# Performance work log

Measured on AMD Instinct MI355X. Metric: run time of the kernel, lower is better.

## Reference

```python
import jax, jax.numpy as jnp
import numpy as np

B, T, NB = 8, 120, 40
VD, WD = 2053, 300
H, E, NH, HD = 512, 256, 8, 64
SEG, NSEG = 12, 10
IDX = np.round(np.linspace(SEG - 1, T - 1, NSEG)).astype(int)  # segment endpoints


def setup_inputs():
    keys = iter(jax.random.split(jax.random.key(0), 64))
    def w(*shape):
        return jax.random.normal(next(keys), shape, jnp.float32) * 0.02
    z = lambda *s: jnp.zeros(s, jnp.float32)
    return dict(
        videos=jax.random.normal(next(keys), (B, T, NB, VD), jnp.float32),
        sub_glove=jax.random.normal(next(keys), (B, WD), jnp.float32),
        obj_glove=jax.random.normal(next(keys), (B, WD), jnp.float32),
        W_ev=w(VD - 5, E), b_ev=z(E),
        W_el=w(5, E), b_el=z(E),
        W_ew=w(WD, E), b_ew=z(E),
        W_sp1=w(2 * E, E), b_sp1=z(E), w_sp2=w(E),
        W_s2o=w(NB, E), b_s2o=z(E),
        W_o2s=w(NB, E), b_o2s=z(E),
        W_tv=w(H, H), b_tv=z(H),
        Wq=w(H, H), bq=z(H), Wk=w(H, H), bk=z(H), Wv=w(H, H), bv=z(H), Wo=w(H, H), bo=z(H),
        g1=jnp.ones(H, jnp.float32), be1=z(H),
        Wf1=w(H, H), bf1=z(H), Wf2=w(H, H), bf2=z(H),
        g2=jnp.ones(H, jnp.float32), be2=z(H),
        W_tr=w(H, H), b_tr=z(H),
        W_tb1=w(2 * H, H), b_tb1=z(H), w_tb2=w(H),
        W_ih=w(4 * H, H), W_hh=w(4 * H, H), b_ih=z(4 * H), b_hh=z(4 * H),
        W_l1=w(2 * H, H), b_l1=z(H), w_l2=w(H),
    )


def reference(videos, sub_glove, obj_glove, W_ev, b_ev, W_el, b_el, W_ew, b_ew,
              W_sp1, b_sp1, w_sp2, W_s2o, b_s2o, W_o2s, b_o2s, W_tv, b_tv,
              Wq, bq, Wk, bk, Wv, bv, Wo, bo, g1, be1, Wf1, bf1, Wf2, bf2, g2, be2,
              W_tr, b_tr, W_tb1, b_tb1, w_tb2, W_ih, W_hh, b_ih, b_hh, W_l1, b_l1, w_l2):
    relu = jax.nn.relu
    # spatialAtt (vectorized over batch; dropout = identity, eval mode)
    ve = relu(videos[..., :VD - 5] @ W_ev + b_ev) + relu(videos[..., VD - 5:] @ W_el + b_el)  # [B,T,NB,E]
    sub_e = relu(sub_glove @ W_ew + b_ew)  # [B,E]
    obj_e = relu(obj_glove @ W_ew + b_ew)

    def attend(word):  # additive attention over bboxes per frame
        wb = jnp.broadcast_to(word[:, None, None, :], ve.shape)
        s = jnp.tanh(jnp.concatenate([ve, wb], -1) @ W_sp1 + b_sp1) @ w_sp2  # [B,T,NB]
        a = jax.nn.softmax(s, -1)
        return jnp.einsum('btn,btne->bte', a, ve), a

    sub_feat, sub_att = attend(sub_e)
    obj_feat, obj_att = attend(obj_e)
    s2o = relu(sub_att @ W_s2o + b_s2o)  # msg_sub2obj on attention weights [B,T,NB]->[B,T,E]
    o2s = relu(obj_att @ W_o2s + b_o2s)
    ori_x = jnp.concatenate([sub_feat + o2s, obj_feat + s2o], -1)  # [B,T,H]
    rel = jnp.concatenate([sub_e, obj_e], -1)[:, None, :]  # [B,1,H]

    def ln(zz, g, b):
        m = zz.mean(-1, keepdims=True)
        v = jnp.mean((zz - m) ** 2, -1, keepdims=True)
        return (zz - m) * jax.lax.rsqrt(v + 1e-5) * g + b

    # transform_visual + 1-layer post-norm TransformerEncoder (relu FFN, dropout=identity)
    x = relu(ori_x @ W_tv + b_tv)
    q = (x @ Wq + bq).reshape(B, T, NH, HD)
    k = (x @ Wk + bk).reshape(B, T, NH, HD)
    v = (x @ Wv + bv).reshape(B, T, NH, HD)
    att = jax.nn.softmax(jnp.einsum('bqhd,bkhd->bhqk', q, k) / np.float32(np.sqrt(HD)), -1)
    ao = jnp.einsum('bhqk,bkhd->bqhd', att, v).reshape(B, T, H) @ Wo + bo
    x = ln(x + ao, g1, be1)
    x = ln(x + relu(x @ Wf1 + bf1) @ Wf2 + bf2, g2, be2)
    within = x  # [B,T,H]

    seg_in = within[:, IDX, :]  # [B,NSEG,H]
    tr = relu(rel @ W_tr + b_tr)
    ctx = jnp.broadcast_to(tr, seg_in.shape)
    beta2 = jax.nn.softmax(jnp.tanh(jnp.concatenate([seg_in, ctx], -1) @ W_tb1 + b_tb1) @ w_tb2, -1)  # [B,NSEG]

    # torch-convention LSTM (gates i,f,g,o); note attention weights are NOT applied to input (vfeat=input)
    def step(carry, xt):
        h, c = carry
        gates = xt @ W_ih.T + h @ W_hh.T + b_ih + b_hh
        i, f, g_, o = jnp.split(gates, 4, -1)
        c = jax.nn.sigmoid(f) * c + jax.nn.sigmoid(i) * jnp.tanh(g_)
        h = jax.nn.sigmoid(o) * jnp.tanh(c)
        return (h, c), h

    (hT, cT), _ = jax.lax.scan(step, (jnp.zeros((B, H), within.dtype), jnp.zeros((B, H), within.dtype)),
                               seg_in.transpose(1, 0, 2))

    ctx2 = jnp.broadcast_to(hT[:, None, :], within.shape)
    beta1 = jax.nn.softmax(jnp.tanh(jnp.concatenate([within, ctx2], -1) @ W_l1 + b_l1) @ w_l2, -1)  # [B,T]
    temp = beta1 + jnp.repeat(beta2, SEG, axis=1)  # temp[:,i] = beta1[:,i] + beta2[:,i//12]
    output = jnp.einsum('bt,bth->bh', temp, within)  # [B,H]
    return output, hT, cT, sub_att, obj_att, beta1, beta2
```

## Files before the change

kernel.cpp:

```cpp
#include <hip/hip_runtime.h>
#include <cstddef>
#include <cstdint>

#define B_ 8
#define T_ 120
#define NB_ 40
#define VD_ 2053
#define E_ 256
#define H_ 512
#define M_ 38400
#define R_ 960

static constexpr size_t OFF_VE    = 0;
static constexpr size_t OFF_SSUB  = OFF_VE + (size_t)M_ * E_;
static constexpr size_t OFF_SOBJ  = OFF_SSUB + M_;
static constexpr size_t OFF_WBS   = OFF_SOBJ + M_;
static constexpr size_t OFF_WBO   = OFF_WBS + B_ * E_;
static constexpr size_t OFF_TBIAS = OFF_WBO + B_ * E_;
static constexpr size_t OFF_ORIX  = OFF_TBIAS + B_ * H_;
static constexpr size_t OFF_X     = OFF_ORIX + (size_t)R_ * H_;
static constexpr size_t OFF_Q     = OFF_X    + (size_t)R_ * H_;
static constexpr size_t OFF_K     = OFF_Q    + (size_t)R_ * H_;
static constexpr size_t OFF_V     = OFF_K    + (size_t)R_ * H_;
static constexpr size_t OFF_AO    = OFF_V    + (size_t)R_ * H_;
static constexpr size_t OFF_ATTN  = OFF_AO   + (size_t)R_ * H_;
static constexpr size_t OFF_X1    = OFF_ATTN + (size_t)R_ * H_;
static constexpr size_t OFF_F1    = OFF_X1   + (size_t)R_ * H_;
static constexpr size_t OFF_F2    = OFF_F1   + (size_t)R_ * H_;
static constexpr size_t OFF_WIN   = OFF_F2   + (size_t)R_ * H_;
static constexpr size_t OFF_WT    = OFF_WIN  + (size_t)R_ * H_;
static constexpr size_t OFF_Z2    = OFF_WT + (size_t)1024 * 2048;
static constexpr size_t OFF_H0    = OFF_Z2 + 128;
static constexpr size_t OFF_HB    = OFF_H0 + 3 * 4096;
static constexpr size_t OFF_L1    = OFF_HB + B_ * H_;
static constexpr size_t OFF_END0  = OFF_L1 + 960;
static constexpr size_t OFF_VEBF  = (OFF_END0 + 3) & ~(size_t)3;
static constexpr size_t OFF_VBF   = OFF_VEBF + (size_t)M_ * E_ / 2;
static constexpr size_t OFF_END   = OFF_VBF + (size_t)M_ * 2048 / 2;

static constexpr size_t O_OUT  = 0;
static constexpr size_t O_HT   = 4096;
static constexpr size_t O_CT   = 8192;
static constexpr size_t O_SATT = 12288;
static constexpr size_t O_OATT = 50688;
static constexpr size_t O_B1   = 89088;
static constexpr size_t O_B2   = 90048;

#define DEVFN __device__ __forceinline__

typedef __attribute__((ext_vector_type(8))) short short8;
typedef __attribute__((ext_vector_type(4))) float f32x4;

DEVFN float sigf(float x) { return 1.0f / (1.0f + __expf(-x)); }

DEVFN float fast_tanh(float x) {
  float e = __expf(2.f * x);
  return 1.f - 2.f / (e + 1.f);
}

DEVFN unsigned short f2bf(float x) {
  unsigned int u = __float_as_uint(x);
  u += 0x7FFFu + ((u >> 16) & 1u);
  return (unsigned short)(u >> 16);
}
DEVFN float bf2f(unsigned short u) { return __uint_as_float((unsigned int)u << 16); }

DEVFN short8 mk8(const float* f) {
  short8 r;
#pragma unroll
  for (int j = 0; j < 8; ++j) r[j] = (short)f2bf(f[j]);
  return r;
}

DEVFN float wredsum(float v) {
#pragma unroll
  for (int m = 32; m; m >>= 1) v += __shfl_xor(v, m);
  return v;
}
DEVFN float wredmax(float v) {
#pragma unroll
  for (int m = 32; m; m >>= 1) v = fmaxf(v, __shfl_xor(v, m));
  return v;
}

__global__ __launch_bounds__(256) void k_zero(float* p, int n) {
  int i = blockIdx.x * 256 + threadIdx.x;
  if (i < n) p[i] = 0.f;
}

__global__ __launch_bounds__(256) void k_small0(
    const float* __restrict__ sub_g, const float* __restrict__ obj_g,
    const float* __restrict__ W_ew, const float* __restrict__ b_ew,
    const float* __restrict__ W_sp1, const float* __restrict__ b_sp1,
    const float* __restrict__ W_tr, const float* __restrict__ b_tr,
    const float* __restrict__ W_tb1, const float* __restrict__ b_tb1,
    float* __restrict__ wbs, float* __restrict__ wbo, float* __restrict__ tbias) {
  int b = blockIdx.x, tid = threadIdx.x;
  __shared__ float sg[300], og[300], se[256], oe[256], trl[512];
  for (int i = tid; i < 300; i += 256) { sg[i] = sub_g[b * 300 + i]; og[i] = obj_g[b * 300 + i]; }
  __syncthreads();
  {
    float a1 = b_ew[tid], a2 = a1;
    for (int w = 0; w < 300; ++w) {
      float we = W_ew[w * 256 + tid];
      a1 += sg[w] * we; a2 += og[w] * we;
    }
    se[tid] = fmaxf(a1, 0.f); oe[tid] = fmaxf(a2, 0.f);
  }
  __syncthreads();
  {
    float a1 = b_sp1[tid], a2 = a1;
    for (int e = 0; e < 256; ++e) {
      float ww = W_sp1[(256 + e) * 256 + tid];
      a1 += se[e] * ww; a2 += oe[e] * ww;
    }
    wbs[b * 256 + tid] = a1; wbo[b * 256 + tid] = a2;
  }
  for (int jj = 0; jj < 2; ++jj) {
    int j = tid + jj * 256;
    float a = b_tr[j];
    for (int i = 0; i < 256; ++i) a += se[i] * W_tr[i * 512 + j];
    for (int i = 0; i < 256; ++i) a += oe[i] * W_tr[(256 + i) * 512 + j];
    trl[j] = fmaxf(a, 0.f);
  }
  __syncthreads();
  for (int jj = 0; jj < 2; ++jj) {
    int j = tid + jj * 256;
    float a = b_tb1[j];
    for (int i = 0; i < 512; ++i) a += trl[i] * W_tb1[(size_t)(512 + i) * 512 + j];
    tbias[b * 512 + j] = a;
  }
}

__global__ __launch_bounds__(256) void k_wconvT(const float* __restrict__ src,
                                                unsigned short* __restrict__ dst,
                                                int K, int N) {
  __shared__ float t[64][65];
  int nblk = N >> 6;
  int kb = blockIdx.x / nblk, nb = blockIdx.x - kb * nblk;
  int tid = threadIdx.x;
#pragma unroll
  for (int i = 0; i < 16; ++i) {
    int idx = tid + 256 * i;
    int r = idx >> 6, c = idx & 63;
    t[r][c] = src[(size_t)(kb * 64 + r) * N + nb * 64 + c];
  }
  __syncthreads();
#pragma unroll
  for (int i = 0; i < 16; ++i) {
    int idx = tid + 256 * i;
    int n = idx >> 6, kk = idx & 63;
    dst[(size_t)(nb * 64 + n) * K + kb * 64 + kk] = f2bf(t[kk][n]);
  }
}

__global__ __launch_bounds__(256) void k_wconv7(
    const float* __restrict__ w0, const float* __restrict__ w1,
    const float* __restrict__ w2, const float* __restrict__ w3,
    const float* __restrict__ w4, const float* __restrict__ w5,
    const float* __restrict__ w6, unsigned short* __restrict__ dstb) {
  __shared__ float t[64][65];
  int wsel = blockIdx.x >> 6, sub = blockIdx.x & 63;
  int kb = sub >> 3, nb = sub & 7;
  const float* src = wsel == 0 ? w0 : wsel == 1 ? w1 : wsel == 2 ? w2
                   : wsel == 3 ? w3 : wsel == 4 ? w4 : wsel == 5 ? w5 : w6;
  unsigned short* dst = dstb + (size_t)wsel * 262144;
  int tid = threadIdx.x;
#pragma unroll
  for (int i = 0; i < 16; ++i) {
    int idx = tid + 256 * i;
    int r = idx >> 6, c = idx & 63;
    t[r][c] = src[(size_t)(kb * 64 + r) * 512 + nb * 64 + c];
  }
  __syncthreads();
#pragma unroll
  for (int i = 0; i < 16; ++i) {
    int idx = tid + 256 * i;
    int n = idx >> 6, kk = idx & 63;
    dst[(size_t)(nb * 64 + n) * 512 + kb * 64 + kk] = f2bf(t[kk][n]);
  }
}

__global__ __launch_bounds__(256) void k_cvt2(const float* __restrict__ a,
                                              const float* __restrict__ b,
                                              unsigned short* __restrict__ da,
                                              unsigned short* __restrict__ db) {
  int i = blockIdx.x * 256 + threadIdx.x;
  const float* s; unsigned short* d; int off;
  if (i < 131072) { s = a; d = da; off = i * 8; }
  else            { s = b; d = db; off = (i - 131072) * 8; }
  float f[8];
#pragma unroll
  for (int j = 0; j < 8; ++j) f[j] = s[off + j];
  *(short8*)(d + off) = mk8(f);
}

__global__ __launch_bounds__(256) void k_v2bf(const float* __restrict__ videos,
                                              unsigned short* __restrict__ vbf) {
  int row = blockIdx.x;
  int c0 = threadIdx.x * 8;
  const float* src = videos + (size_t)row * VD_ + c0;
  float f[8];
#pragma unroll
  for (int j = 0; j < 8; ++j) f[j] = src[j];
  *(short8*)(vbf + (size_t)row * 2048 + c0) = mk8(f);
}

__global__ __launch_bounds__(512) void k_gemm_ve_m97(
    const unsigned short* __restrict__ vbf, const float* __restrict__ videos,
    const unsigned short* __restrict__ wtbf, const float* __restrict__ bev,
    const float* __restrict__ Wel, const float* __restrict__ bel,
    unsigned short* __restrict__ vebf) {
  __shared__ __align__(16) unsigned short lds[20480];
  int tid = threadIdx.x;
  int rowbase = blockIdx.x * 64;
  int lane = tid & 63, wid = tid >> 6;
  int l16 = lane & 15, lk = lane >> 4;

  const unsigned short* sp[5];
  int dst[5];
#pragma unroll
  for (int i = 0; i < 5; ++i) {
    int g = tid + 512 * i;
    if (g < 512) {
      int row = g >> 3, kc = g & 7;
      sp[i] = vbf + (size_t)(rowbase + row) * 2048 + kc * 8;
      dst[i] = row * 64 + ((kc ^ (row & 7)) * 8);
    } else {
      int n = (g - 512) >> 3, kc = (g - 512) & 7;
      sp[i] = wtbf + (size_t)n * 2048 + kc * 8;
      dst[i] = 4096 + n * 64 + ((kc ^ (n & 7)) * 8);
    }
  }
  short8 st[5];
#pragma unroll
  for (int i = 0; i < 5; ++i) st[i] = *(const short8*)(sp[i]);

  f32x4 acc[4][2] = {};
  for (int k0 = 0; k0 < 2048; k0 += 64) {
    __syncthreads();
#pragma unroll
    for (int i = 0; i < 5; ++i) *(short8*)(lds + dst[i]) = st[i];
    __syncthreads();
    int kn = (k0 + 64 < 2048) ? k0 + 64 : 0;
#pragma unroll
    for (int i = 0; i < 5; ++i) st[i] = *(const short8*)(sp[i] + kn);
#pragma unroll
    for (int kk = 0; kk < 2; ++kk) {
      short8 a8[4], b8[2];
#pragma unroll
      for (int fm = 0; fm < 4; ++fm) {
        int row = fm * 16 + l16;
        a8[fm] = *(const short8*)(lds + row * 64 + (((kk * 4 + lk) ^ (row & 7)) * 8));
      }
#pragma unroll
      for (int fn = 0; fn < 2; ++fn) {
        int n = wid * 32 + fn * 16 + l16;
        b8[fn] = *(const short8*)(lds + 4096 + n * 64 + (((kk * 4 + lk) ^ (n & 7)) * 8));
      }
#pragma unroll
      for (int fm = 0; fm < 4; ++fm)
#pragma unroll
        for (int fn = 0; fn < 2; ++fn)
          acc[fm][fn] = __builtin_amdgcn_mfma_f32_16x16x32_bf16(
              a8[fm], b8[fn], acc[fm][fn], 0, 0, 0);
    }
  }
  float bevv[2], belv[2], w5[5][2];
#pragma unroll
  for (int fn = 0; fn < 2; ++fn) {
    int col = wid * 32 + fn * 16 + l16;
    bevv[fn] = bev[col]; belv[fn] = bel[col];
#pragma unroll
    for (int kk = 0; kk < 5; ++kk) w5[kk][fn] = Wel[kk * 256 + col];
  }
#pragma unroll
  for (int fm = 0; fm < 4; ++fm) {
#pragma unroll
    for (int r = 0; r < 4; ++r) {
      int grow = rowbase + fm * 16 + lk * 4 + r;
      const float* vt = videos + (size_t)grow * VD_ + 2048;
      float t0 = vt[0], t1 = vt[1], t2 = vt[2], t3 = vt[3], t4 = vt[4];
      unsigned short* vob = vebf + (size_t)grow * 256;
#pragma unroll
      for (int fn = 0; fn < 2; ++fn) {
        int col = wid * 32 + fn * 16 + l16;
        float s2 = belv[fn] + t0 * w5[0][fn] + t1 * w5[1][fn] + t2 * w5[2][fn] +
                   t3 * w5[3][fn] + t4 * w5[4][fn];
        float vvv = fmaxf(acc[fm][fn][r] + bevv[fn], 0.f) + fmaxf(s2, 0.f);
        vob[col] = f2bf(vvv);
      }
    }
  }
}

__global__ __launch_bounds__(256) void k_score_bf(
    const unsigned short* __restrict__ vebf, const unsigned short* __restrict__ wsp1,
    const float* __restrict__ w_sp2, const float* __restrict__ wbs,
    const float* __restrict__ wbo, float* __restrict__ s_sub,
    float* __restrict__ s_obj) {
  __shared__ float reds[4][64], redo_[4][64];
  int tid = threadIdx.x;
  int rowbase = blockIdx.x * 64;
  int lane = tid & 63, wid = tid >> 6;
  int l16 = lane & 15, lk = lane >> 4;
  const unsigned short* ap[4];
  const unsigned short* bp[4];
#pragma unroll
  for (int fm = 0; fm < 4; ++fm)
    ap[fm] = vebf + (size_t)(rowbase + fm * 16 + l16) * 256 + lk * 8;
#pragma unroll
  for (int fn = 0; fn < 4; ++fn)
    bp[fn] = wsp1 + (size_t)(wid * 64 + fn * 16 + l16) * 256 + lk * 8;
  f32x4 acc[4][4] = {};
#pragma unroll 2
  for (int k0 = 0; k0 < 256; k0 += 32) {
    short8 a8[4], b8[4];
#pragma unroll
    for (int fm = 0; fm < 4; ++fm) a8[fm] = *(const short8*)(ap[fm] + k0);
#pragma unroll
    for (int fn = 0; fn < 4; ++fn) b8[fn] = *(const short8*)(bp[fn] + k0);
#pragma unroll
    for (int fm = 0; fm < 4; ++fm)
#pragma unroll
      for (int fn = 0; fn < 4; ++fn)
        acc[fm][fn] = __builtin_amdgcn_mfma_f32_16x16x32_bf16(
            a8[fm], b8[fn], acc[fm][fn], 0, 0, 0);
  }
  int b = rowbase / 4800;
  float w2[4], bs[4], bo[4];
#pragma unroll
  for (int fn = 0; fn < 4; ++fn) {
    int col = wid * 64 + fn * 16 + l16;
    w2[fn] = w_sp2[col];
    bs[fn] = wbs[b * 256 + col];
    bo[fn] = wbo[b * 256 + col];
  }
  float ps[4][4], po[4][4];
#pragma unroll
  for (int fm = 0; fm < 4; ++fm)
#pragma unroll
    for (int r = 0; r < 4; ++r) {
      float aps = 0, apo = 0;
#pragma unroll
      for (int fn = 0; fn < 4; ++fn) {
        float t = acc[fm][fn][r];
        aps += fast_tanh(t + bs[fn]) * w2[fn];
        apo += fast_tanh(t + bo[fn]) * w2[fn];
      }
      ps[fm][r] = aps;
      po[fm][r] = apo;
    }
#pragma unroll
  for (int m = 1; m < 16; m <<= 1) {
#pragma unroll
    for (int fm = 0; fm < 4; ++fm)
#pragma unroll
      for (int r = 0; r < 4; ++r) {
        ps[fm][r] += __shfl_xor(ps[fm][r], m);
        po[fm][r] += __shfl_xor(po[fm][r], m);
      }
  }
  if (l16 == 0) {
#pragma unroll
    for (int fm = 0; fm < 4; ++fm)
#pragma unroll
      for (int r = 0; r < 4; ++r) {
        int row = fm * 16 + lk * 4 + r;
        reds[wid][row] = ps[fm][r];
        redo_[wid][row] = po[fm][r];
      }
  }
  __syncthreads();
  if (tid < 64) {
    float s1 = reds[0][tid] + reds[1][tid] + reds[2][tid] + reds[3][tid];
    float s2 = redo_[0][tid] + redo_[1][tid] + redo_[2][tid] + redo_[3][tid];
    s_sub[rowbase + tid] = s1;
    s_obj[rowbase + tid] = s2;
  }
}

__global__ __launch_bounds__(256) void k_attend_bf(
    const float* __restrict__ s_sub, const float* __restrict__ s_obj,
    const unsigned short* __restrict__ vebf, const float* __restrict__ W_s2o,
    const float* __restrict__ b_s2o, const float* __restrict__ W_o2s,
    const float* __restrict__ b_o2s, float* __restrict__ out_satt,
    float* __restrict__ out_oatt, float* __restrict__ orix) {
  int row = blockIdx.x;
  int tid = threadIdx.x;
  __shared__ float alds[2][40];
  int wv = tid >> 6, lane = tid & 63;
  if (wv < 2) {
    const float* sarr = (wv ? s_obj : s_sub) + row * 40;
    float v = (lane < 40) ? sarr[lane] : -1e30f;
    float mx = wredmax(v);
    float e = (lane < 40) ? __expf(v - mx) : 0.f;
    float sm = wredsum(e);
    float p = e / sm;
    if (lane < 40) {
// ... 262 lines not shown
    av[fm] = base < 80;
    int grow = base + l16;
    int s = grow >> 3, b = grow & 7;
    ap[fm] = av[fm] ? (win + (size_t)(b * 120 + 11 + 12 * s) * 512 + lk * 8)
                    : win;
  }
  const unsigned short* bp[2];
#pragma unroll
  for (int fn = 0; fn < 2; ++fn)
    bp[fn] = wih + (size_t)(nt * 64 + wcol * 32 + fn * 16 + l16) * 512 + lk * 8;
  f32x4 acc[2][2] = {};
  for (int k0 = 0; k0 < 512; k0 += 64) {
#pragma unroll
    for (int kk = 0; kk < 2; ++kk) {
      int ko = k0 + kk * 32;
      short8 a8[2], b8[2];
#pragma unroll
      for (int fm = 0; fm < 2; ++fm) {
        if (av[fm]) {
          float4 x = *(const float4*)(ap[fm] + ko);
          float4 y = *(const float4*)(ap[fm] + ko + 4);
          float f[8] = {x.x, x.y, x.z, x.w, y.x, y.y, y.z, y.w};
          a8[fm] = mk8(f);
        } else {
          a8[fm] = short8{0, 0, 0, 0, 0, 0, 0, 0};
        }
      }
#pragma unroll
      for (int fn = 0; fn < 2; ++fn) b8[fn] = *(const short8*)(bp[fn] + ko);
#pragma unroll
      for (int fm = 0; fm < 2; ++fm)
#pragma unroll
        for (int fn = 0; fn < 2; ++fn)
          acc[fm][fn] = __builtin_amdgcn_mfma_f32_16x16x32_bf16(
              a8[fm], b8[fn], acc[fm][fn], 0, 0, 0);
    }
  }
#pragma unroll
  for (int fn = 0; fn < 2; ++fn) {
    int cg = nt * 64 + wcol * 32 + fn * 16 + l16;
    float bv = b_ih[cg] + b_hh[cg];
#pragma unroll
    for (int fm = 0; fm < 2; ++fm) {
      if (!av[fm]) continue;
#pragma unroll
      for (int r = 0; r < 4; ++r) {
        int grow = mt * 64 + wrow * 32 + fm * 16 + lk * 4 + r;
        if (grow < 80) gx[(size_t)grow * 2048 + cg] = acc[fm][fn][r] + bv;
      }
    }
  }
}

__global__ __launch_bounds__(128) void k_lstm_step(
    const float* __restrict__ hin, const unsigned short* __restrict__ whh,
    const float* __restrict__ gx, int s, float* __restrict__ hout,
    float* __restrict__ c_st) {
  int jb = blockIdx.x;
  int tid = threadIdx.x;
  int lane = tid & 63, kw = tid >> 6;
  int l16 = lane & 15, lk = lane >> 4;
  const float* ap = hin + (size_t)l16 * 512 + kw * 256 + lk * 8;
  const unsigned short* bp[4];
#pragma unroll
  for (int fn = 0; fn < 4; ++fn)
    bp[fn] = whh + (size_t)(fn * 512 + jb * 16 + l16) * 512 + kw * 256 + lk * 8;
  f32x4 acc[4] = {};
  for (int k0 = 0; k0 < 256; k0 += 64) {
#pragma unroll
    for (int kk = 0; kk < 2; ++kk) {
      int ko = k0 + kk * 32;
      float4 x = *(const float4*)(ap + ko);
      float4 y = *(const float4*)(ap + ko + 4);
      float f[8] = {x.x, x.y, x.z, x.w, y.x, y.y, y.z, y.w};
      short8 a8 = mk8(f);
#pragma unroll
      for (int fn = 0; fn < 4; ++fn) {
        short8 b8 = *(const short8*)(bp[fn] + ko);
        acc[fn] = __builtin_amdgcn_mfma_f32_16x16x32_bf16(a8, b8, acc[fn], 0, 0, 0);
      }
    }
  }
  __shared__ float part[4][64][4];
  if (kw == 1) {
#pragma unroll
    for (int fn = 0; fn < 4; ++fn)
#pragma unroll
      for (int r = 0; r < 4; ++r) part[fn][lane][r] = acc[fn][r];
  }
  __syncthreads();
  if (kw == 0 && lk < 2) {
    int j = jb * 16 + l16;
#pragma unroll
    for (int r = 0; r < 4; ++r) {
      int b = lk * 4 + r;
      const float* g = gx + (size_t)(s * 8 + b) * 2048;
      float gi = acc[0][r] + part[0][lane][r] + g[j];
      float gf = acc[1][r] + part[1][lane][r] + g[512 + j];
      float gg = acc[2][r] + part[2][lane][r] + g[1024 + j];
      float go = acc[3][r] + part[3][lane][r] + g[1536 + j];
      float c = sigf(gf) * c_st[b * 512 + j] + sigf(gi) * fast_tanh(gg);
      c_st[b * 512 + j] = c;
      hout[b * 512 + j] = sigf(go) * fast_tanh(c);
    }
  }
}

__global__ __launch_bounds__(256) void k_mha(const float* __restrict__ qb,
                                             const float* __restrict__ kb,
                                             const float* __restrict__ vb,
                                             float* __restrict__ ao) {
  int bh = blockIdx.x & 63, qc = blockIdx.x >> 6;
  int b = bh >> 3, h = bh & 7;
  __shared__ float ks[120 * 65];
  __shared__ float vs[120 * 65];
  __shared__ float ps[4][128];
  int tid = threadIdx.x;
  for (int i = 0; i < 30; ++i) {
    int idx = tid + 256 * i;
    int t = idx >> 6, d = idx & 63;
    size_t g = (size_t)(b * 120 + t) * 512 + h * 64 + d;
    ks[t * 65 + d] = kb[g];
    vs[t * 65 + d] = vb[g];
  }
  __syncthreads();
  int wv = tid >> 6, lane = tid & 63;
  for (int i = qc * 30 + wv; i < qc * 30 + 30; i += 4) {
    const float* qrow = qb + (size_t)(b * 120 + i) * 512 + h * 64;
    float s1 = 0, s2 = 0;
    for (int d = 0; d < 64; ++d) {
      float qd = qrow[d];
      s1 += qd * ks[lane * 65 + d];
      if (lane < 56) s2 += qd * ks[(lane + 64) * 65 + d];
    }
    s1 *= 0.125f;
    s2 *= 0.125f;
    if (lane >= 56) s2 = -1e30f;
    float mx = wredmax(fmaxf(s1, s2));
    float e1 = __expf(s1 - mx);
    float e2 = (lane < 56) ? __expf(s2 - mx) : 0.f;
    float sm = wredsum(e1 + e2);
    ps[wv][lane] = e1;
    ps[wv][64 + lane] = e2;
    float o = 0;
    for (int j = 0; j < 120; ++j) o += ps[wv][j] * vs[j * 65 + lane];
    ao[(size_t)(b * 120 + i) * 512 + h * 64 + lane] = o / sm;
  }
}

__global__ __launch_bounds__(256) void k_ln(const float* __restrict__ a,
                                            const float* __restrict__ bsrc,
                                            const float* __restrict__ g,
                                            const float* __restrict__ be,
                                            float* __restrict__ out) {
  int row = blockIdx.x * 4 + (threadIdx.x >> 6);
  int lane = threadIdx.x & 63;
  const float* pa = a + (size_t)row * 512;
  const float* pb = bsrc + (size_t)row * 512;
  float z[8];
  float s = 0;
#pragma unroll
  for (int ii = 0; ii < 8; ++ii) {
    int e = lane + 64 * ii;
    z[ii] = pa[e] + pb[e];
    s += z[ii];
  }
  float mean = wredsum(s) * (1.f / 512.f);
  float v = 0;
#pragma unroll
  for (int ii = 0; ii < 8; ++ii) {
    float d = z[ii] - mean;
    v += d * d;
  }
  float rstd = rsqrtf(wredsum(v) * (1.f / 512.f) + 1e-5f);
#pragma unroll
  for (int ii = 0; ii < 8; ++ii) {
    int e = lane + 64 * ii;
    out[(size_t)row * 512 + e] = (z[ii] - mean) * rstd * g[e] + be[e];
  }
}

__global__ __launch_bounds__(256) void k_hbias(const float* __restrict__ hT,
                                               const float* __restrict__ W_l1,
                                               const float* __restrict__ b_l1,
                                               float* __restrict__ hb) {
  int b = blockIdx.x >> 1, half = blockIdx.x & 1;
  int tid = threadIdx.x;
  __shared__ float hl[512];
  for (int i = tid; i < 512; i += 256) hl[i] = hT[b * 512 + i];
  __syncthreads();
  int j = half * 256 + tid;
  float a = b_l1[j];
  for (int i = 0; i < 512; ++i) a += hl[i] * W_l1[(size_t)(512 + i) * 512 + j];
  hb[b * 512 + j] = a;
}

__global__ __launch_bounds__(256) void k_beta2(
    const float* __restrict__ within, const float* __restrict__ W_tb1,
    const float* __restrict__ w_tb2, const float* __restrict__ tbias,
    float* __restrict__ z2) {
  int bid = blockIdx.x;
  int b = bid / 10, si = bid - b * 10;
  int trow = b * 120 + 11 + 12 * si;
  int tid = threadIdx.x;
  __shared__ float xr[512];
  __shared__ float red[256];
  for (int i = tid; i < 512; i += 256) xr[i] = within[(size_t)trow * 512 + i];
  __syncthreads();
  float val = 0;
  for (int jj = 0; jj < 2; ++jj) {
    int j = tid + jj * 256;
    float a = tbias[b * 512 + j];
    for (int i = 0; i < 512; ++i) a += xr[i] * W_tb1[(size_t)i * 512 + j];
    val += fast_tanh(a) * w_tb2[j];
  }
  red[tid] = val;
  __syncthreads();
  for (int s = 128; s; s >>= 1) {
    if (tid < s) red[tid] += red[tid + s];
    __syncthreads();
  }
  if (tid == 0) z2[bid] = red[0];
}

__global__ __launch_bounds__(256) void k_beta1(
    const float* __restrict__ within, const float* __restrict__ W_l1,
    const float* __restrict__ w_l2, const float* __restrict__ hb,
    float* __restrict__ l1) {
  int bid = blockIdx.x;
  int r0 = bid * 4;
  int b = r0 / 120;
  int tid = threadIdx.x;
  __shared__ float xr[4][512];
  __shared__ float red[4][256];
  for (int i = tid; i < 2048; i += 256) xr[i >> 9][i & 511] = within[(size_t)r0 * 512 + i];
  __syncthreads();
  float v[4] = {0, 0, 0, 0};
  for (int jj = 0; jj < 2; ++jj) {
    int j = tid + jj * 256;
    float hbv = hb[b * 512 + j];
    float a0 = hbv, a1 = hbv, a2 = hbv, a3 = hbv;
    for (int i = 0; i < 512; ++i) {
      float ww = W_l1[(size_t)i * 512 + j];
      a0 += xr[0][i] * ww;
      a1 += xr[1][i] * ww;
      a2 += xr[2][i] * ww;
      a3 += xr[3][i] * ww;
    }
    float wl = w_l2[j];
    v[0] += fast_tanh(a0) * wl;
    v[1] += fast_tanh(a1) * wl;
    v[2] += fast_tanh(a2) * wl;
    v[3] += fast_tanh(a3) * wl;
  }
#pragma unroll
  for (int r = 0; r < 4; ++r) red[r][tid] = v[r];
  __syncthreads();
  for (int s = 128; s; s >>= 1) {
    if (tid < s)
      for (int r = 0; r < 4; ++r) red[r][tid] += red[r][tid + s];
    __syncthreads();
  }
  if (tid < 4) l1[r0 + tid] = red[tid][0];
}

__global__ __launch_bounds__(256) void k_final(
    const float* __restrict__ l1, const float* __restrict__ z2,
    const float* __restrict__ within, const float* __restrict__ hT,
    const float* __restrict__ cT, float* __restrict__ dout) {
  int b = blockIdx.x;
  int tid = threadIdx.x;
  __shared__ float temp[120];
  __shared__ float b2[10];
  int wv = tid >> 6, lane = tid & 63;
  if (wv == 1) {
    float v = (lane < 10) ? z2[b * 10 + lane] : -1e30f;
    float mx = wredmax(v);
    float e = (lane < 10) ? __expf(v - mx) : 0.f;
    float sm = wredsum(e);
    if (lane < 10) {
      float p = e / sm;
      b2[lane] = p;
      dout[O_B2 + b * 10 + lane] = p;
    }
  }
  if (wv == 0) {
    float v1 = l1[b * 120 + lane];
    float v2 = (lane + 64 < 120) ? l1[b * 120 + 64 + lane] : -1e30f;
    float mx = wredmax(fmaxf(v1, v2));
    float e1 = __expf(v1 - mx);
    float e2 = (lane + 64 < 120) ? __expf(v2 - mx) : 0.f;
    float sm = wredsum(e1 + e2);
    float p1 = e1 / sm;
    dout[O_B1 + b * 120 + lane] = p1;
    temp[lane] = p1;
    if (lane + 64 < 120) {
      float p2 = e2 / sm;
      dout[O_B1 + b * 120 + 64 + lane] = p2;
      temp[64 + lane] = p2;
    }
  }
  __syncthreads();
  for (int t = tid; t < 120; t += 256) temp[t] += b2[t / 12];
  __syncthreads();
  for (int hh = tid; hh < 512; hh += 256) {
    float o = 0;
    for (int t = 0; t < 120; ++t) o += temp[t] * within[(size_t)(b * 120 + t) * 512 + hh];
    dout[O_OUT + b * 512 + hh] = o;
    dout[O_HT + b * 512 + hh] = hT[b * 512 + hh];
    dout[O_CT + b * 512 + hh] = cT[b * 512 + hh];
  }
}

extern "C" void kernel_launch(void* const* d_in, const int* in_sizes, int n_in,
                              void* d_out, int out_size, void* d_ws, size_t ws_size,
                              hipStream_t stream) {
  const float* videos = (const float*)d_in[0];
  const float* sub_g  = (const float*)d_in[1];
  const float* obj_g  = (const float*)d_in[2];
  const float* W_ev   = (const float*)d_in[3];
  const float* b_ev   = (const float*)d_in[4];
  const float* W_el   = (const float*)d_in[5];
  const float* b_el   = (const float*)d_in[6];
  const float* W_ew   = (const float*)d_in[7];
  const float* b_ew   = (const float*)d_in[8];
  const float* W_sp1  = (const float*)d_in[9];
  const float* b_sp1  = (const float*)d_in[10];
  const float* w_sp2  = (const float*)d_in[11];
  const float* W_s2o  = (const float*)d_in[12];
  const float* b_s2o  = (const float*)d_in[13];
  const float* W_o2s  = (const float*)d_in[14];
  const float* b_o2s  = (const float*)d_in[15];
  const float* W_tv   = (const float*)d_in[16];
  const float* b_tv   = (const float*)d_in[17];
  const float* Wq     = (const float*)d_in[18];
  const float* bq     = (const float*)d_in[19];
  const float* Wk     = (const float*)d_in[20];
  const float* bk     = (const float*)d_in[21];
  const float* Wv     = (const float*)d_in[22];
  const float* bv     = (const float*)d_in[23];
  const float* Wo     = (const float*)d_in[24];
  const float* bo     = (const float*)d_in[25];
  const float* g1     = (const float*)d_in[26];
  const float* be1    = (const float*)d_in[27];
  const float* Wf1    = (const float*)d_in[28];
  const float* bf1    = (const float*)d_in[29];
  const float* Wf2    = (const float*)d_in[30];
  const float* bf2    = (const float*)d_in[31];
  const float* g2     = (const float*)d_in[32];
  const float* be2    = (const float*)d_in[33];
  const float* W_tr   = (const float*)d_in[34];
  const float* b_tr   = (const float*)d_in[35];
  const float* W_tb1  = (const float*)d_in[36];
  const float* b_tb1  = (const float*)d_in[37];
  const float* w_tb2  = (const float*)d_in[38];
  const float* W_ih   = (const float*)d_in[39];
  const float* W_hh   = (const float*)d_in[40];
  const float* b_ih   = (const float*)d_in[41];
  const float* b_hh   = (const float*)d_in[42];
  const float* W_l1   = (const float*)d_in[43];
  const float* b_l1   = (const float*)d_in[44];
  const float* w_l2   = (const float*)d_in[45];

  float* out = (float*)d_out;
  float* w = (float*)d_ws;

  float* ve_p   = w + OFF_VE;
  float* ssub_p = w + OFF_SSUB;
  float* sobj_p = w + OFF_SOBJ;
  float* wbs_p  = w + OFF_WBS;
  float* wbo_p  = w + OFF_WBO;
  float* tb_p   = w + OFF_TBIAS;
  float* orix_p = w + OFF_ORIX;
  float* x_p    = w + OFF_X;
  float* q_p    = w + OFF_Q;
  float* k_p    = w + OFF_K;
  float* v_p    = w + OFF_V;
  float* ao_p   = w + OFF_AO;
  float* attn_p = w + OFF_ATTN;
  float* x1_p   = w + OFF_X1;
  float* f1_p   = w + OFF_F1;
  float* f2_p   = w + OFF_F2;
  float* win_p  = w + OFF_WIN;
  float* z2_p   = w + OFF_Z2;
  float* h_p    = w + OFF_H0;
  float* c_p    = h_p + 2 * 4096;
  float* hb_p   = w + OFF_HB;
  float* l1_p   = w + OFF_L1;

  unsigned short* wtbase = (unsigned short*)(w + OFF_WT);
  unsigned short* wevbf = wtbase;
  unsigned short* w7bf  = wtbase + 524288;
  unsigned short* wtvbf = w7bf;
  unsigned short* wqbf  = w7bf + 1 * 262144;
  unsigned short* wobf  = w7bf + 4 * 262144;
  unsigned short* wf1bf = w7bf + 5 * 262144;
  unsigned short* wf2bf = w7bf + 6 * 262144;
  unsigned short* wsp1bf = w7bf + 7 * 262144;
  float* gx_p = w + OFF_Q;
  unsigned short* wihbf = (unsigned short*)(w + OFF_Q + 163840);
  unsigned short* whhbf = (unsigned short*)(w + OFF_Q + 688128);
  unsigned short* vebf_p = (unsigned short*)(w + OFF_VEBF);
  unsigned short* vbf_p  = (unsigned short*)(w + OFF_VBF);
  const bool big = ws_size >= (size_t)OFF_END * 4;

  k_zero<<<48, 256, 0, stream>>>(h_p, 3 * 4096);
  k_small0<<<8, 256, 0, stream>>>(sub_g, obj_g, W_ew, b_ew, W_sp1, b_sp1, W_tr,
                                  b_tr, W_tb1, b_tb1, wbs_p, wbo_p, tb_p);
  k_wconvT<<<128, 256, 0, stream>>>(W_ev, wevbf, 2048, 256);
  k_wconv7<<<448, 256, 0, stream>>>(W_tv, Wq, Wk, Wv, Wo, Wf1, Wf2, w7bf);
  if (big) {
    k_wconvT<<<16, 256, 0, stream>>>(W_sp1, wsp1bf, 256, 256);
    k_v2bf<<<38400, 256, 0, stream>>>(videos, vbf_p);
    k_gemm_ve_m97<<<600, 512, 0, stream>>>(vbf_p, videos, wevbf, b_ev, W_el,
                                           b_el, vebf_p);
    k_score_bf<<<600, 256, 0, stream>>>(vebf_p, wsp1bf, w_sp2, wbs_p, wbo_p,
                                        ssub_p, sobj_p);
    k_attend_bf<<<960, 256, 0, stream>>>(ssub_p, sobj_p, vebf_p, W_s2o, b_s2o,
                                         W_o2s, b_o2s, out + O_SATT,
                                         out + O_OATT, orix_p);
  } else {
    k_gemm_ve_mfma<<<600, 256, 0, stream>>>(videos, wevbf, b_ev, W_el, b_el, ve_p);
    k_score<<<1200, 256, 0, stream>>>(ve_p, W_sp1, w_sp2, wbs_p, wbo_p, ssub_p, sobj_p);
    k_attend<<<960, 256, 0, stream>>>(ssub_p, sobj_p, ve_p, W_s2o, b_s2o, W_o2s,
                                      b_o2s, out + O_SATT, out + O_OATT, orix_p);
  }
  k_gemm_h<<<120, 256, 0, stream>>>(orix_p, wtvbf, b_tv, b_tv, b_tv, x_p, 8, 1);
  k_gemm_h<<<360, 256, 0, stream>>>(x_p, wqbf, bq, bk, bv, q_p, 24, 0);
  k_mha<<<256, 256, 0, stream>>>(q_p, k_p, v_p, ao_p);
  k_gemm_h<<<120, 256, 0, stream>>>(ao_p, wobf, bo, bo, bo, attn_p, 8, 0);
  k_ln<<<240, 256, 0, stream>>>(x_p, attn_p, g1, be1, x1_p);
  k_gemm_h<<<120, 256, 0, stream>>>(x1_p, wf1bf, bf1, bf1, bf1, f1_p, 8, 1);
  k_gemm_h<<<120, 256, 0, stream>>>(f1_p, wf2bf, bf2, bf2, bf2, f2_p, 8, 0);
  k_ln<<<240, 256, 0, stream>>>(x1_p, f2_p, g2, be2, win_p);
  k_cvt2<<<1024, 256, 0, stream>>>(W_ih, W_hh, wihbf, whhbf);
  k_xproj<<<64, 256, 0, stream>>>(win_p, wihbf, b_ih, b_hh, gx_p);
  k_beta2<<<80, 256, 0, stream>>>(win_p, W_tb1, w_tb2, tb_p, z2_p);
  for (int s = 0; s < 10; ++s) {
    float* hin = h_p + (s & 1) * 4096;
    float* hout = h_p + ((s & 1) ^ 1) * 4096;
    k_lstm_step<<<32, 128, 0, stream>>>(hin, whhbf, gx_p, s, hout, c_p);
  }
  k_hbias<<<16, 256, 0, stream>>>(h_p, W_l1, b_l1, hb_p);
  k_beta1<<<240, 256, 0, stream>>>(win_p, W_l1, w_l2, hb_p, l1_p);
  k_final<<<8, 256, 0, stream>>>(l1_p, z2_p, win_p, h_p, c_p, out);
}
```

Baseline: 704.9 us.

## Fuse video bf16 conversion into VE GEMM, merge weight prep, MFMA beta1

```diff
diff --git a/kernel.cpp b/kernel.cpp
--- a/kernel.cpp
+++ b/kernel.cpp
@@ -34,9 +34,12 @@
 static constexpr size_t OFF_HB    = OFF_H0 + 3 * 4096;
 static constexpr size_t OFF_L1    = OFF_HB + B_ * H_;
 static constexpr size_t OFF_END0  = OFF_L1 + 960;
-static constexpr size_t OFF_VEBF  = (OFF_END0 + 3) & ~(size_t)3;
-static constexpr size_t OFF_VBF   = OFF_VEBF + (size_t)M_ * E_ / 2;
-static constexpr size_t OFF_END   = OFF_VBF + (size_t)M_ * 2048 / 2;
+static constexpr size_t OFF_WIH   = (OFF_END0 + 3) & ~(size_t)3;
+static constexpr size_t OFF_WHH   = OFF_WIH + 524288;
+static constexpr size_t OFF_WL1B  = OFF_WHH + 524288;
+static constexpr size_t OFF_WINBF = OFF_WL1B + 131072;
+static constexpr size_t OFF_VEBF  = OFF_WINBF + 245760;
+static constexpr size_t OFF_END   = OFF_VEBF + (size_t)M_ * E_ / 2;
 
 static constexpr size_t O_OUT  = 0;
 static constexpr size_t O_HT   = 4096;
@@ -129,6 +132,92 @@
     float a = b_tb1[j];
     for (int i = 0; i < 512; ++i) a += trl[i] * W_tb1[(size_t)(512 + i) * 512 + j];
     tbias[b * 512 + j] = a;
+  }
+}
+
+__global__ __launch_bounds__(256) void k_wprep(
+    const float* __restrict__ W_ev, const float* __restrict__ W_tv,
+    const float* __restrict__ Wq, const float* __restrict__ Wk,
+    const float* __restrict__ Wv, const float* __restrict__ Wo,
+    const float* __restrict__ Wf1, const float* __restrict__ Wf2,
+    const float* __restrict__ W_sp1, const float* __restrict__ W_l1,
+    const float* __restrict__ W_ih, const float* __restrict__ W_hh,
+    unsigned short* __restrict__ wevbf, unsigned short* __restrict__ w7bf,
+    unsigned short* __restrict__ wsp1bf, unsigned short* __restrict__ wl1bf,
+    unsigned short* __restrict__ wihbf, unsigned short* __restrict__ whhbf,
+    float* __restrict__ hz) {
+  int bid = blockIdx.x, tid = threadIdx.x;
+  __shared__ float t[64][65];
+  if (bid < 128) {
+    int kb = bid >> 2, nb = bid & 3;
+#pragma unroll
+    for (int i = 0; i < 16; ++i) {
+      int idx = tid + 256 * i; int r = idx >> 6, c = idx & 63;
+      t[r][c] = W_ev[(size_t)(kb * 64 + r) * 256 + nb * 64 + c];
+    }
+    __syncthreads();
+#pragma unroll
+    for (int i = 0; i < 16; ++i) {
+      int idx = tid + 256 * i; int n = idx >> 6, kk = idx & 63;
+      wevbf[(size_t)(nb * 64 + n) * 2048 + kb * 64 + kk] = f2bf(t[kk][n]);
+    }
+  } else if (bid < 576) {
+    int b2 = bid - 128;
+    int wsel = b2 >> 6, sub = b2 & 63;
+    int kb = sub >> 3, nb = sub & 7;
+    const float* src = wsel == 0 ? W_tv : wsel == 1 ? Wq : wsel == 2 ? Wk
+                     : wsel == 3 ? Wv : wsel == 4 ? Wo : wsel == 5 ? Wf1 : Wf2;
+    unsigned short* dst = w7bf + (size_t)wsel * 262144;
+#pragma unroll
+    for (int i = 0; i < 16; ++i) {
+      int idx = tid + 256 * i; int r = idx >> 6, c = idx & 63;
+      t[r][c] = src[(size_t)(kb * 64 + r) * 512 + nb * 64 + c];
+    }
+    __syncthreads();
+#pragma unroll
+    for (int i = 0; i < 16; ++i) {
+      int idx = tid + 256 * i; int n = idx >> 6, kk = idx & 63;
+      dst[(size_t)(nb * 64 + n) * 512 + kb * 64 + kk] = f2bf(t[kk][n]);
+    }
+  } else if (bid < 592) {
+    int b2 = bid - 576;
+    int kb = b2 >> 2, nb = b2 & 3;
+#pragma unroll
+    for (int i = 0; i < 16; ++i) {
+      int idx = tid + 256 * i; int r = idx >> 6, c = idx & 63;
+      t[r][c] = W_sp1[(size_t)(kb * 64 + r) * 256 + nb * 64 + c];
+    }
+    __syncthreads();
+#pragma unroll
+    for (int i = 0; i < 16; ++i) {
+      int idx = tid + 256 * i; int n = idx >> 6, kk = idx & 63;
+      wsp1bf[(size_t)(nb * 64 + n) * 256 + kb * 64 + kk] = f2bf(t[kk][n]);
+    }
+  } else if (bid < 656) {
+    int b2 = bid - 592;
+    int kb = b2 >> 3, nb = b2 & 7;
+#pragma unroll
+    for (int i = 0; i < 16; ++i) {
+      int idx = tid + 256 * i; int r = idx >> 6, c = idx & 63;
+      t[r][c] = W_l1[(size_t)(kb * 64 + r) * 512 + nb * 64 + c];
+    }
+    __syncthreads();
+#pragma unroll
+    for (int i = 0; i < 16; ++i) {
+      int idx = tid + 256 * i; int n = idx >> 6, kk = idx & 63;
+      wl1bf[(size_t)(nb * 64 + n) * 512 + kb * 64 + kk] = f2bf(t[kk][n]);
+    }
+  } else if (bid < 1680) {
+    int i = (bid - 656) * 256 + tid;
+    const float* s; unsigned short* d; int off;
+    if (i < 131072) { s = W_ih; d = wihbf; off = i * 8; }
+    else            { s = W_hh; d = whhbf; off = (i - 131072) * 8; }
+    float f[8];
+#pragma unroll
+    for (int j = 0; j < 8; ++j) f[j] = s[off + j];
+    *(short8*)(d + off) = mk8(f);
+  } else {
+    for (int i = tid; i < 12288; i += 256) hz[i] = 0.f;
   }
 }
 
@@ -195,56 +284,48 @@
   *(short8*)(d + off) = mk8(f);
 }
 
-__global__ __launch_bounds__(256) void k_v2bf(const float* __restrict__ videos,
-                                              unsigned short* __restrict__ vbf) {
-  int row = blockIdx.x;
-  int c0 = threadIdx.x * 8;
-  const float* src = videos + (size_t)row * VD_ + c0;
-  float f[8];
-#pragma unroll
-  for (int j = 0; j < 8; ++j) f[j] = src[j];
-  *(short8*)(vbf + (size_t)row * 2048 + c0) = mk8(f);
-}
-
 __global__ __launch_bounds__(512) void k_gemm_ve_m97(
-    const unsigned short* __restrict__ vbf, const float* __restrict__ videos,
-    const unsigned short* __restrict__ wtbf, const float* __restrict__ bev,
-    const float* __restrict__ Wel, const float* __restrict__ bel,
-    unsigned short* __restrict__ vebf) {
+    const float* __restrict__ videos, const unsigned short* __restrict__ wtbf,
+    const float* __restrict__ bev, const float* __restrict__ Wel,
+    const float* __restrict__ bel, unsigned short* __restrict__ vebf) {
   __shared__ __align__(16) unsigned short lds[20480];
   int tid = threadIdx.x;
   int rowbase = blockIdx.x * 64;
   int lane = tid & 63, wid = tid >> 6;
   int l16 = lane & 15, lk = lane >> 4;
 
-  const unsigned short* sp[5];
-  int dst[5];
-#pragma unroll
-  for (int i = 0; i < 5; ++i) {
+  int arow = tid >> 3, akc = tid & 7;
+  const float* apA = videos + (size_t)(rowbase + arow) * VD_ + akc * 8;
+  int dstA = arow * 64 + ((akc ^ (arow & 7)) * 8);
+  const unsigned short* spB[4];
+  int dstB[4];
+#pragma unroll
+  for (int i = 0; i < 4; ++i) {
     int g = tid + 512 * i;
-    if (g < 512) {
-      int row = g >> 3, kc = g & 7;
-      sp[i] = vbf + (size_t)(rowbase + row) * 2048 + kc * 8;
-      dst[i] = row * 64 + ((kc ^ (row & 7)) * 8);
-    } else {
-      int n = (g - 512) >> 3, kc = (g - 512) & 7;
-      sp[i] = wtbf + (size_t)n * 2048 + kc * 8;
-      dst[i] = 4096 + n * 64 + ((kc ^ (n & 7)) * 8);
-    }
-  }
-  short8 st[5];
-#pragma unroll
-  for (int i = 0; i < 5; ++i) st[i] = *(const short8*)(sp[i]);
+    int n = g >> 3, kc = g & 7;
+    spB[i] = wtbf + (size_t)n * 2048 + kc * 8;
+    dstB[i] = 4096 + n * 64 + ((kc ^ (n & 7)) * 8);
+  }
+  float fa[8];
+  short8 stB[4];
+#pragma unroll
+  for (int j = 0; j < 8; ++j) fa[j] = apA[j];
+#pragma unroll
+  for (int i = 0; i < 4; ++i) stB[i] = *(const short8*)(spB[i]);
 
   f32x4 acc[4][2] = {};
   for (int k0 = 0; k0 < 2048; k0 += 64) {
+    short8 ha = mk8(fa);
     __syncthreads();
-#pragma unroll
-    for (int i = 0; i < 5; ++i) *(short8*)(lds + dst[i]) = st[i];
+    *(short8*)(lds + dstA) = ha;
+#pragma unroll
+    for (int i = 0; i < 4; ++i) *(short8*)(lds + dstB[i]) = stB[i];
     __syncthreads();
     int kn = (k0 + 64 < 2048) ? k0 + 64 : 0;
 #pragma unroll
-    for (int i = 0; i < 5; ++i) st[i] = *(const short8*)(sp[i] + kn);
+    for (int j = 0; j < 8; ++j) fa[j] = apA[kn + j];
+#pragma unroll
+    for (int i = 0; i < 4; ++i) stB[i] = *(const short8*)(spB[i] + kn);
 #pragma unroll
     for (int kk = 0; kk < 2; ++kk) {
       short8 a8[4], b8[2];
@@ -813,7 +894,8 @@
                                             const float* __restrict__ bsrc,
                                             const float* __restrict__ g,
                                             const float* __restrict__ be,
-                                            float* __restrict__ out) {
+                                            float* __restrict__ out,
+                                            unsigned short* __restrict__ bfout) {
   int row = blockIdx.x * 4 + (threadIdx.x >> 6);
   int lane = threadIdx.x & 63;
   const float* pa = a + (size_t)row * 512;
@@ -837,7 +919,9 @@
 #pragma unroll
   for (int ii = 0; ii < 8; ++ii) {
     int e = lane + 64 * ii;
-    out[(size_t)row * 512 + e] = (z[ii] - mean) * rstd * g[e] + be[e];
+    float val = (z[ii] - mean) * rstd * g[e] + be[e];
+    out[(size_t)row * 512 + e] = val;
+    if (bfout) bfout[(size_t)row * 512 + e] = f2bf(val);
   }
 }
 
@@ -882,6 +966,70 @@
     __syncthreads();
   }
   if (tid == 0) z2[bid] = red[0];
+}
+
+__global__ __launch_bounds__(256) void k_beta1_bf(
+    const unsigned short* __restrict__ winbf, const unsigned short* __restrict__ wl1bf,
+    const float* __restrict__ w_l2, const float* __restrict__ hb,
+    float* __restrict__ l1) {
+  __shared__ float reds[4][64];
+  int tid = threadIdx.x;
+  int rowbase = blockIdx.x * 64;
+  int lane = tid & 63, wid = tid >> 6;
+  int l16 = lane & 15, lk = lane >> 4;
+  const unsigned short* ap[4];
+#pragma unroll
+  for (int fm = 0; fm < 4; ++fm)
+    ap[fm] = winbf + (size_t)(rowbase + fm * 16 + l16) * 512 + lk * 8;
+  float ps[4][4] = {};
+#pragma unroll
+  for (int cs = 0; cs < 2; ++cs) {
+    const unsigned short* bp[4];
+#pragma unroll
+    for (int fn = 0; fn < 4; ++fn)
+      bp[fn] = wl1bf + (size_t)(cs * 256 + wid * 64 + fn * 16 + l16) * 512 + lk * 8;
+    f32x4 acc[4][4] = {};
+    for (int k0 = 0; k0 < 512; k0 += 32) {
+      short8 a8[4], b8[4];
+#pragma unroll
+      for (int fm = 0; fm < 4; ++fm) a8[fm] = *(const short8*)(ap[fm] + k0);
+#pragma unroll
+      for (int fn = 0; fn < 4; ++fn) b8[fn] = *(const short8*)(bp[fn] + k0);
+#pragma unroll
+      for (int fm = 0; fm < 4; ++fm)
+#pragma unroll
+        for (int fn = 0; fn < 4; ++fn)
+          acc[fm][fn] = __builtin_amdgcn_mfma_f32_16x16x32_bf16(
+              a8[fm], b8[fn], acc[fm][fn], 0, 0, 0);
+    }
+#pragma unroll
+    for (int fm = 0; fm < 4; ++fm)
+#pragma unroll
+      for (int r = 0; r < 4; ++r) {
+        int grow = rowbase + fm * 16 + lk * 4 + r;
+        int b = grow / 120;
+#pragma unroll
+        for (int fn = 0; fn < 4; ++fn) {
+          int col = cs * 256 + wid * 64 + fn * 16 + l16;
+          ps[fm][r] += fast_tanh(acc[fm][fn][r] + hb[b * 512 + col]) * w_l2[col];
+        }
+      }
+  }
+#pragma unroll
+  for (int m = 1; m < 16; m <<= 1)
+#pragma unroll
+    for (int fm = 0; fm < 4; ++fm)
+#pragma unroll
+      for (int r = 0; r < 4; ++r) ps[fm][r] += __shfl_xor(ps[fm][r], m);
+  if (l16 == 0) {
+#pragma unroll
+    for (int fm = 0; fm < 4; ++fm)
+#pragma unroll
+      for (int r = 0; r < 4; ++r) reds[wid][fm * 16 + lk * 4 + r] = ps[fm][r];
+  }
+  __syncthreads();
+  if (tid < 64)
+    l1[rowbase + tid] = reds[0][tid] + reds[1][tid] + reds[2][tid] + reds[3][tid];
 }
 
 __global__ __launch_bounds__(256) void k_beta1(
@@ -1058,51 +1206,75 @@
   unsigned short* wf1bf = w7bf + 5 * 262144;
   unsigned short* wf2bf = w7bf + 6 * 262144;
   unsigned short* wsp1bf = w7bf + 7 * 262144;
+  unsigned short* wihbf  = (unsigned short*)(w + OFF_WIH);
+  unsigned short* whhbf  = (unsigned short*)(w + OFF_WHH);
+  unsigned short* wl1bf  = (unsigned short*)(w + OFF_WL1B);
+  unsigned short* winbf_p = (unsigned short*)(w + OFF_WINBF);
+  unsigned short* vebf_p = (unsigned short*)(w + OFF_VEBF);
   float* gx_p = w + OFF_Q;
-  unsigned short* wihbf = (unsigned short*)(w + OFF_Q + 163840);
-  unsigned short* whhbf = (unsigned short*)(w + OFF_Q + 688128);
-  unsigned short* vebf_p = (unsigned short*)(w + OFF_VEBF);
-  unsigned short* vbf_p  = (unsigned short*)(w + OFF_VBF);
   const bool big = ws_size >= (size_t)OFF_END * 4;
 
-  k_zero<<<48, 256, 0, stream>>>(h_p, 3 * 4096);
-  k_small0<<<8, 256, 0, stream>>>(sub_g, obj_g, W_ew, b_ew, W_sp1, b_sp1, W_tr,
-                                  b_tr, W_tb1, b_tb1, wbs_p, wbo_p, tb_p);
-  k_wconvT<<<128, 256, 0, stream>>>(W_ev, wevbf, 2048, 256);
-  k_wconv7<<<448, 256, 0, stream>>>(W_tv, Wq, Wk, Wv, Wo, Wf1, Wf2, w7bf);
   if (big) {
-    k_wconvT<<<16, 256, 0, stream>>>(W_sp1, wsp1bf, 256, 256);
-    k_v2bf<<<38400, 256, 0, stream>>>(videos, vbf_p);
-    k_gemm_ve_m97<<<600, 512, 0, stream>>>(vbf_p, videos, wevbf, b_ev, W_el,
-                                           b_el, vebf_p);
+    k_wprep<<<1681, 256, 0, stream>>>(W_ev, W_tv, Wq, Wk, Wv, Wo, Wf1, Wf2,
+                                      W_sp1, W_l1, W_ih, W_hh, wevbf, w7bf,
+                                      wsp1bf, wl1bf, wihbf, whhbf, h_p);
+    k_small0<<<8, 256, 0, stream>>>(sub_g, obj_g, W_ew, b_ew, W_sp1, b_sp1,
+                                    W_tr, b_tr, W_tb1, b_tb1, wbs_p, wbo_p, tb_p);
+    k_gemm_ve_m97<<<600, 512, 0, stream>>>(videos, wevbf, b_ev, W_el, b_el,
+                                           vebf_p);
     k_score_bf<<<600, 256, 0, stream>>>(vebf_p, wsp1bf, w_sp2, wbs_p, wbo_p,
                                         ssub_p, sobj_p);
     k_attend_bf<<<960, 256, 0, stream>>>(ssub_p, sobj_p, vebf_p, W_s2o, b_s2o,
                                          W_o2s, b_o2s, out + O_SATT,
                                          out + O_OATT, orix_p);
+    k_gemm_h<<<120, 256, 0, stream>>>(orix_p, wtvbf, b_tv, b_tv, b_tv, x_p, 8, 1);
+    k_gemm_h<<<360, 256, 0, stream>>>(x_p, wqbf, bq, bk, bv, q_p, 24, 0);
+    k_mha<<<256, 256, 0, stream>>>(q_p, k_p, v_p, ao_p);
+    k_gemm_h<<<120, 256, 0, stream>>>(ao_p, wobf, bo, bo, bo, attn_p, 8, 0);
+    k_ln<<<240, 256, 0, stream>>>(x_p, attn_p, g1, be1, x1_p, nullptr);
+    k_gemm_h<<<120, 256, 0, stream>>>(x1_p, wf1bf, bf1, bf1, bf1, f1_p, 8, 1);
+    k_gemm_h<<<120, 256, 0, stream>>>(f1_p, wf2bf, bf2, bf2, bf2, f2_p, 8, 0);
+    k_ln<<<240, 256, 0, stream>>>(x1_p, f2_p, g2, be2, win_p, winbf_p);
+    k_xproj<<<64, 256, 0, stream>>>(win_p, wihbf, b_ih, b_hh, gx_p);
+    k_beta2<<<80, 256, 0, stream>>>(win_p, W_tb1, w_tb2, tb_p, z2_p);
+    for (int s = 0; s < 10; ++s) {
+      float* hin = h_p + (s & 1) * 4096;
+      float* hout = h_p + ((s & 1) ^ 1) * 4096;
+      k_lstm_step<<<32, 128, 0, stream>>>(hin, whhbf, gx_p, s, hout, c_p);
+    }
+    k_hbias<<<16, 256, 0, stream>>>(h_p, W_l1, b_l1, hb_p);
+    k_beta1_bf<<<15, 256, 0, stream>>>(winbf_p, wl1bf, w_l2, hb_p, l1_p);
+    k_final<<<8, 256, 0, stream>>>(l1_p, z2_p, win_p, h_p, c_p, out);
   } else {
+    unsigned short* wihbf_a = (unsigned short*)(w + OFF_Q + 163840);
+    unsigned short* whhbf_a = (unsigned short*)(w + OFF_Q + 688128);
+    k_zero<<<48, 256, 0, stream>>>(h_p, 3 * 4096);
+    k_small0<<<8, 256, 0, stream>>>(sub_g, obj_g, W_ew, b_ew, W_sp1, b_sp1,
+                                    W_tr, b_tr, W_tb1, b_tb1, wbs_p, wbo_p, tb_p);
+    k_wconvT<<<128, 256, 0, stream>>>(W_ev, wevbf, 2048, 256);
+    k_wconv7<<<448, 256, 0, stream>>>(W_tv, Wq, Wk, Wv, Wo, Wf1, Wf2, w7bf);
     k_gemm_ve_mfma<<<600, 256, 0, stream>>>(videos, wevbf, b_ev, W_el, b_el, ve_p);
     k_score<<<1200, 256, 0, stream>>>(ve_p, W_sp1, w_sp2, wbs_p, wbo_p, ssub_p, sobj_p);
     k_attend<<<960, 256, 0, stream>>>(ssub_p, sobj_p, ve_p, W_s2o, b_s2o, W_o2s,
                                       b_o2s, out + O_SATT, out + O_OATT, orix_p);
-  }
-  k_gemm_h<<<120, 256, 0, stream>>>(orix_p, wtvbf, b_tv, b_tv, b_tv, x_p, 8, 1);
-  k_gemm_h<<<360, 256, 0, stream>>>(x_p, wqbf, bq, bk, bv, q_p, 24, 0);
-  k_mha<<<256, 256, 0, stream>>>(q_p, k_p, v_p, ao_p);
-  k_gemm_h<<<120, 256, 0, stream>>>(ao_p, wobf, bo, bo, bo, attn_p, 8, 0);
-  k_ln<<<240, 256, 0, stream>>>(x_p, attn_p, g1, be1, x1_p);
-  k_gemm_h<<<120, 256, 0, stream>>>(x1_p, wf1bf, bf1, bf1, bf1, f1_p, 8, 1);
-  k_gemm_h<<<120, 256, 0, stream>>>(f1_p, wf2bf, bf2, bf2, bf2, f2_p, 8, 0);
-  k_ln<<<240, 256, 0, stream>>>(x1_p, f2_p, g2, be2, win_p);
-  k_cvt2<<<1024, 256, 0, stream>>>(W_ih, W_hh, wihbf, whhbf);
-  k_xproj<<<64, 256, 0, stream>>>(win_p, wihbf, b_ih, b_hh, gx_p);
-  k_beta2<<<80, 256, 0, stream>>>(win_p, W_tb1, w_tb2, tb_p, z2_p);
-  for (int s = 0; s < 10; ++s) {
-    float* hin = h_p + (s & 1) * 4096;
-    float* hout = h_p + ((s & 1) ^ 1) * 4096;
-    k_lstm_step<<<32, 128, 0, stream>>>(hin, whhbf, gx_p, s, hout, c_p);
-  }
-  k_hbias<<<16, 256, 0, stream>>>(h_p, W_l1, b_l1, hb_p);
-  k_beta1<<<240, 256, 0, stream>>>(win_p, W_l1, w_l2, hb_p, l1_p);
-  k_final<<<8, 256, 0, stream>>>(l1_p, z2_p, win_p, h_p, c_p, out);
-}
+    k_gemm_h<<<120, 256, 0, stream>>>(orix_p, wtvbf, b_tv, b_tv, b_tv, x_p, 8, 1);
+    k_gemm_h<<<360, 256, 0, stream>>>(x_p, wqbf, bq, bk, bv, q_p, 24, 0);
+    k_mha<<<256, 256, 0, stream>>>(q_p, k_p, v_p, ao_p);
+    k_gemm_h<<<120, 256, 0, stream>>>(ao_p, wobf, bo, bo, bo, attn_p, 8, 0);
+    k_ln<<<240, 256, 0, stream>>>(x_p, attn_p, g1, be1, x1_p, nullptr);
+    k_gemm_h<<<120, 256, 0, stream>>>(x1_p, wf1bf, bf1, bf1, bf1, f1_p, 8, 1);
+    k_gemm_h<<<120, 256, 0, stream>>>(f1_p, wf2bf, bf2, bf2, bf2, f2_p, 8, 0);
+    k_ln<<<240, 256, 0, stream>>>(x1_p, f2_p, g2, be2, win_p, nullptr);
+    k_cvt2<<<1024, 256, 0, stream>>>(W_ih, W_hh, wihbf_a, whhbf_a);
+    k_xproj<<<64, 256, 0, stream>>>(win_p, wihbf_a, b_ih, b_hh, gx_p);
+    k_beta2<<<80, 256, 0, stream>>>(win_p, W_tb1, w_tb2, tb_p, z2_p);
+    for (int s = 0; s < 10; ++s) {
+      float* hin = h_p + (s & 1) * 4096;
+      float* hout = h_p + ((s & 1) ^ 1) * 4096;
+      k_lstm_step<<<32, 128, 0, stream>>>(hin, whhbf_a, gx_p, s, hout, c_p);
+    }
+    k_hbias<<<16, 256, 0, stream>>>(h_p, W_l1, b_l1, hb_p);
+    k_beta1<<<240, 256, 0, stream>>>(win_p, W_l1, w_l2, hb_p, l1_p);
+    k_final<<<8, 256, 0, stream>>>(l1_p, z2_p, win_p, h_p, c_p, out);
+  }
+}
```

Result: faster. 661.0 us (-6.2%).
